# Performance work log

Hardware: AMD Instinct MI355X
Metric: run time of the kernel (lower is better)

The kernel has to match this reference:

```python
import jax, jax.numpy as jnp
import numpy as np

H = 8          # n_channels
NEIGHBORS = 5


def setup_inputs() -> dict:
    key = jax.random.key(0)
    k1, k2 = jax.random.split(key)
    B, N, C = 8, 1024, 256
    x = jax.random.normal(k1, (B, N, C), dtype=jnp.float32)
    # torch Linear weight: [out_features, in_features] = [2*H*C, C]
    W_qk = jax.random.normal(k2, (2 * H * C, C), dtype=jnp.float32) * (C ** -0.5)
    return {"x": x, "W_qk": W_qk}


def _forward(x, W_qk):
    B, N, C = x.shape
    scale = C ** -0.5
    qk = (x @ W_qk.T).reshape(B, N, 2, H, C).transpose(2, 0, 3, 1, 4)
    q, k = qk[0], qk[1]                              # [B,H,N,C]
    attn = jax.nn.softmax(jnp.einsum('bhnc,bhmc->bhnm', q, k) * scale, axis=-1)

    # clip(): top-k on detached channel-summed attention
    sum_edge = jnp.sum(jax.lax.stop_gradient(attn), axis=1)   # [B,N,N]
    _, index = jax.lax.top_k(sum_edge, NEIGHBORS)             # [B,N,NEIGHBORS]
    # Faithful to source: every mask row gets 1 at the union of ALL rows'
    # top-k indices (inner loop iterates over all rows of `inds`), plus eye(N).
    flat_idx = index.reshape(B, N * NEIGHBORS)                # [B, N*nb]
    col_mask = jnp.zeros((B, N), dtype=attn.dtype).at[
        jnp.arange(B)[:, None], flat_idx].set(1.0)            # [B,N]
    mask = jnp.maximum(jnp.eye(N, dtype=attn.dtype)[None], col_mask[:, None, :])  # [B,N,N]

    new_edge = mask[:, None] * attn                           # [B,H,N,N]

    # norm_edge(): row norm, then col norm, then row @ col^T
    norm_row = new_edge / (jnp.sum(new_edge, axis=-1, keepdims=True) + 1e-16)
    norm_col = norm_row / (jnp.sum(norm_row, axis=-2, keepdims=True) + 1e-16)
    return jnp.einsum('bhnm,bhkm->bhnk', norm_row, norm_col)  # [B,H,N,N]


def reference(x, W_qk):
    return _forward(x, W_qk)
```

## Files before the change

kernel.cpp:

```cpp
#include <hip/hip_runtime.h>
#include <hip/hip_bf16.h>
#include <cstdint>
#include <cstddef>

#define BB 8
#define HH 8
#define NN 1024
#define CC 256
#define OUTCH 4096

typedef __attribute__((ext_vector_type(8))) __bf16 bf16x8;
typedef __attribute__((ext_vector_type(4))) __bf16 bf16x4;
typedef __attribute__((ext_vector_type(4))) float f32x4;

__device__ inline void async16(const void* g, void* l)
{
  __builtin_amdgcn_global_load_lds(
      reinterpret_cast<const __attribute__((address_space(1))) unsigned int*>(
          reinterpret_cast<uintptr_t>(g)),
      reinterpret_cast<__attribute__((address_space(3))) unsigned int*>(
          reinterpret_cast<uintptr_t>(l)),
      16, 0, 0);
}

__device__ inline float waveMax(float v) {
#pragma unroll
  for (int o = 32; o > 0; o >>= 1) v = fmaxf(v, __shfl_xor(v, o, 64));
  return v;
}
__device__ inline float waveSum(float v) {
#pragma unroll
  for (int o = 32; o > 0; o >>= 1) v += __shfl_xor(v, o, 64);
  return v;
}

__global__ __launch_bounds__(256) void split_kernel(const float* __restrict__ in,
                                                    __bf16* __restrict__ hi,
                                                    __bf16* __restrict__ lo, int n4)
{
  const int i = blockIdx.x * 256 + threadIdx.x;
  if (i >= n4) return;
  const float4 v = ((const float4*)in)[i];
  bf16x4 h, l;
  h.x = (__bf16)v.x; l.x = (__bf16)(v.x - (float)h.x);
  h.y = (__bf16)v.y; l.y = (__bf16)(v.y - (float)h.y);
  h.z = (__bf16)v.z; l.z = (__bf16)(v.z - (float)h.z);
  h.w = (__bf16)v.w; l.w = (__bf16)(v.w - (float)h.w);
  ((bf16x4*)hi)[i] = h;
  ((bf16x4*)lo)[i] = l;
}

__global__ __launch_bounds__(256) void xw_mfma_kernel(
    const __bf16* __restrict__ Ah, const __bf16* __restrict__ Al,
    const __bf16* __restrict__ Bh, const __bf16* __restrict__ Bl,
    __bf16* __restrict__ Chi, __bf16* __restrict__ Clo)
{
  __shared__ __bf16 AsH[128 * 32], AsL[128 * 32], BsH[128 * 32], BsL[128 * 32];

  const int tid = threadIdx.x, lane = tid & 63, wid = tid >> 6;
  const int wr = wid >> 1, wc = wid & 1;
  const int bM = blockIdx.y * 128, bN = blockIdx.x * 128;

  const int srow = wid * 16 + (lane >> 2);
  const int scol = (lane & 3) * 8;
  const __bf16* gAh = Ah + (size_t)(bM + srow) * CC + scol;
  const __bf16* gAl = Al + (size_t)(bM + srow) * CC + scol;
  const __bf16* gBh = Bh + (size_t)(bN + srow) * CC + scol;
  const __bf16* gBl = Bl + (size_t)(bN + srow) * CC + scol;
  char* lAh = (char*)AsH + wid * 16 * 64;
  char* lAl = (char*)AsL + wid * 16 * 64;
  char* lBh = (char*)BsH + wid * 16 * 64;
  char* lBl = (char*)BsL + wid * 16 * 64;

  f32x4 acc[4][4];
  const f32x4 z = {0.f, 0.f, 0.f, 0.f};
#pragma unroll
  for (int m = 0; m < 4; ++m)
#pragma unroll
    for (int n = 0; n < 4; ++n) acc[m][n] = z;

  for (int k0 = 0; k0 < CC; k0 += 32) {
    async16(gAh + k0, lAh); async16(gAh + k0 + 64 * CC, lAh + 64 * 64);
    async16(gAl + k0, lAl); async16(gAl + k0 + 64 * CC, lAl + 64 * 64);
    async16(gBh + k0, lBh); async16(gBh + k0 + 64 * CC, lBh + 64 * 64);
    async16(gBl + k0, lBl); async16(gBl + k0 + 64 * CC, lBl + 64 * 64);
    __syncthreads();

    bf16x8 ah[4], al[4], bh_[4], bl_[4];
    const int fb = (lane & 15) * 64 + (lane >> 4) * 16;
#pragma unroll
    for (int m = 0; m < 4; ++m) {
      ah[m] = *(const bf16x8*)((const char*)AsH + (wr * 64 + m * 16) * 64 + fb);
      al[m] = *(const bf16x8*)((const char*)AsL + (wr * 64 + m * 16) * 64 + fb);
    }
#pragma unroll
    for (int n = 0; n < 4; ++n) {
      bh_[n] = *(const bf16x8*)((const char*)BsH + (wc * 64 + n * 16) * 64 + fb);
      bl_[n] = *(const bf16x8*)((const char*)BsL + (wc * 64 + n * 16) * 64 + fb);
    }
#pragma unroll
    for (int m = 0; m < 4; ++m)
#pragma unroll
      for (int n = 0; n < 4; ++n) {
        acc[m][n] = __builtin_amdgcn_mfma_f32_16x16x32_bf16(al[m], bh_[n], acc[m][n], 0, 0, 0);
        acc[m][n] = __builtin_amdgcn_mfma_f32_16x16x32_bf16(ah[m], bl_[n], acc[m][n], 0, 0, 0);
        acc[m][n] = __builtin_amdgcn_mfma_f32_16x16x32_bf16(ah[m], bh_[n], acc[m][n], 0, 0, 0);
      }
    __syncthreads();
  }

  const int fr = lane & 15;
  const int fq = lane >> 4;
#pragma unroll
  for (int m = 0; m < 4; ++m) {
    const int row0 = bM + wr * 64 + m * 16 + fq * 4;
#pragma unroll
    for (int n = 0; n < 4; ++n) {
      const int col = bN + wc * 64 + n * 16 + fr;
#pragma unroll
      for (int r = 0; r < 4; ++r) {
        const float v = acc[m][n][r];
        const __bf16 h = (__bf16)v;
        const __bf16 l = (__bf16)(v - (float)h);
        Chi[(size_t)(row0 + r) * OUTCH + col] = h;
        Clo[(size_t)(row0 + r) * OUTCH + col] = l;
      }
    }
  }
}

__global__ __launch_bounds__(256) void qkt_mfma_kernel(
    const __bf16* __restrict__ Qh, const __bf16* __restrict__ Ql,
    float* __restrict__ outall)
{
  const int f = blockIdx.x;
  const int xcd = f & 7;
  const int g = f >> 3;
  const int bh = xcd + 8 * (g >> 6);
  const int tile = g & 63;
  const int b = bh >> 3, h = bh & 7;
  const size_t qoff = (size_t)b * NN * OUTCH + (size_t)h * CC;
  const size_t koff = qoff + 2048;
  float* C = outall + ((size_t)bh << 20);

  __shared__ __bf16 AsH[128 * 32], AsL[128 * 32], BsH[128 * 32], BsL[128 * 32];

  const int tid = threadIdx.x, lane = tid & 63, wid = tid >> 6;
  const int wr = wid >> 1, wc = wid & 1;
  const int bM = (tile >> 3) * 128, bN = (tile & 7) * 128;

  const int srow = wid * 16 + (lane >> 2);
  const int scol = (lane & 3) * 8;
  const __bf16* gAh = Qh + qoff + (size_t)(bM + srow) * OUTCH + scol;
  const __bf16* gAl = Ql + qoff + (size_t)(bM + srow) * OUTCH + scol;
  const __bf16* gBh = Qh + koff + (size_t)(bN + srow) * OUTCH + scol;
  const __bf16* gBl = Ql + koff + (size_t)(bN + srow) * OUTCH + scol;
  char* lAh = (char*)AsH + wid * 16 * 64;
  char* lAl = (char*)AsL + wid * 16 * 64;
  char* lBh = (char*)BsH + wid * 16 * 64;
  char* lBl = (char*)BsL + wid * 16 * 64;

  f32x4 acc[4][4];
  const f32x4 z = {0.f, 0.f, 0.f, 0.f};
#pragma unroll
  for (int m = 0; m < 4; ++m)
#pragma unroll
    for (int n = 0; n < 4; ++n) acc[m][n] = z;

  for (int k0 = 0; k0 < CC; k0 += 32) {
    async16(gAh + k0, lAh); async16(gAh + k0 + (size_t)64 * OUTCH, lAh + 64 * 64);
    async16(gAl + k0, lAl); async16(gAl + k0 + (size_t)64 * OUTCH, lAl + 64 * 64);
    async16(gBh + k0, lBh); async16(gBh + k0 + (size_t)64 * OUTCH, lBh + 64 * 64);
    async16(gBl + k0, lBl); async16(gBl + k0 + (size_t)64 * OUTCH, lBl + 64 * 64);
    __syncthreads();

    bf16x8 ah[4], al[4], bh_[4], bl_[4];
    const int fb = (lane & 15) * 64 + (lane >> 4) * 16;
#pragma unroll
    for (int m = 0; m < 4; ++m) {
      ah[m] = *(const bf16x8*)((const char*)AsH + (wr * 64 + m * 16) * 64 + fb);
      al[m] = *(const bf16x8*)((const char*)AsL + (wr * 64 + m * 16) * 64 + fb);
    }
#pragma unroll
    for (int n = 0; n < 4; ++n) {
      bh_[n] = *(const bf16x8*)((const char*)BsH + (wc * 64 + n * 16) * 64 + fb);
      bl_[n] = *(const bf16x8*)((const char*)BsL + (wc * 64 + n * 16) * 64 + fb);
    }
#pragma unroll
    for (int m = 0; m < 4; ++m)
#pragma unroll
      for (int n = 0; n < 4; ++n) {
        acc[m][n] = __builtin_amdgcn_mfma_f32_16x16x32_bf16(al[m], bh_[n], acc[m][n], 0, 0, 0);
        acc[m][n] = __builtin_amdgcn_mfma_f32_16x16x32_bf16(ah[m], bl_[n], acc[m][n], 0, 0, 0);
        acc[m][n] = __builtin_amdgcn_mfma_f32_16x16x32_bf16(ah[m], bh_[n], acc[m][n], 0, 0, 0);
      }
    __syncthreads();
  }

  const int fr = lane & 15;
  const int fq = lane >> 4;
#pragma unroll
  for (int m = 0; m < 4; ++m) {
    const int row0 = bM + wr * 64 + m * 16 + fq * 4;
#pragma unroll
    for (int n = 0; n < 4; ++n) {
      const int col = bN + wc * 64 + n * 16 + fr;
#pragma unroll
      for (int r = 0; r < 4; ++r)
        C[(size_t)(row0 + r) * NN + col] = acc[m][n][r] * 0.0625f;
    }
  }
}

__global__ __launch_bounds__(256) void softmax_se_kernel(const float* __restrict__ logits,
                                                         __bf16* __restrict__ attnb,
                                                         float* __restrict__ se)
{
  const int bn = blockIdx.x;
  const int b = bn >> 10;
  const int n = bn & 1023;
  const int t = threadIdx.x;
  const int lane = t & 63, wv = t >> 6;
  __shared__ float wred[4];
  float4 acc = make_float4(0.f, 0.f, 0.f, 0.f);

#pragma unroll 1
  for (int h = 0; h < HH; ++h) {
    const size_t rowbase = (((size_t)(b * HH + h) << 10) + n) << 10;
    const float* ar = logits + rowbase;
    __bf16* arb = attnb + rowbase;
    float4 x = *(const float4*)(ar + (t << 2));
    float mx = waveMax(fmaxf(fmaxf(x.x, x.y), fmaxf(x.z, x.w)));
    if (lane == 0) wred[wv] = mx;
    __syncthreads();
    const float M = fmaxf(fmaxf(wred[0], wred[1]), fmaxf(wred[2], wred[3]));
    __syncthreads();

    float e0 = expf(x.x - M), e1 = expf(x.y - M), e2 = expf(x.z - M), e3 = expf(x.w - M);
    float s = waveSum(e0 + e1 + e2 + e3);
    if (lane == 0) wred[wv] = s;
    __syncthreads();
    const float inv = 1.0f / (wred[0] + wred[1] + wred[2] + wred[3]);

    const float o0 = e0 * inv, o1 = e1 * inv, o2 = e2 * inv, o3 = e3 * inv;
    bf16x4 ob; ob.x = (__bf16)o0; ob.y = (__bf16)o1; ob.z = (__bf16)o2; ob.w = (__bf16)o3;
    *(bf16x4*)(arb + (t << 2)) = ob;
    acc.x += o0; acc.y += o1; acc.z += o2; acc.w += o3;
    __syncthreads();
  }
  *(float4*)(se + (size_t)bn * NN + (t << 2)) = acc;
}

__global__ __launch_bounds__(256) void topk_kernel(const float* __restrict__ se,
                                                   float* __restrict__ colmask)
{
  const int bn = blockIdx.x;
  const int b = bn >> 10;
  const int t = threadIdx.x;
  __shared__ float vals[NN];
  __shared__ unsigned long long red[256];
  const float* rowp = se + (size_t)bn * NN;
  for (int i = t; i < NN; i += 256) vals[i] = rowp[i];
  __syncthreads();

  for (int it = 0; it < 5; ++it) {
    unsigned long long best = 0ull;
    for (int i = t; i < NN; i += 256) {
      const float v = vals[i];
      if (v >= 0.f) {
        unsigned long long key =
            ((unsigned long long)__float_as_uint(v) << 32) | (unsigned)(NN - 1 - i);
        if (key > best) best = key;
      }
    }
    red[t] = best; __syncthreads();
    for (int s = 128; s > 0; s >>= 1) {
      if (t < s) red[t] = red[t] > red[t+s] ? red[t] : red[t+s];
      __syncthreads();
    }
    if (t == 0) {
      const int idx = NN - 1 - (int)(red[0] & 0xFFFFFFFFull);
      colmask[b * NN + idx] = 1.0f;
      vals[idx] = -1.0f;
    }
    __syncthreads();
  }
}

__global__ __launch_bounds__(256) void cs_rs_kernel(const __bf16* __restrict__ attnb,
                                                    const float* __restrict__ colmask,
                                                    float* __restrict__ inv_rs,
                                                    float* __restrict__ part)
{
  const int bh = blockIdx.y;
  const int b = bh >> 3;
  const int chunk = blockIdx.x;
  const int t = threadIdx.x, lane = t & 63, wv = t >> 6;
  const __bf16* ab = attnb + ((size_t)bh << 20);
  const float* cm = colmask + b * NN;
  const int c0 = lane * 16;

  float cmv[16];
#pragma unroll
  for (int q = 0; q < 4; ++q) {
    const float4 c4 = *(const float4*)(cm + c0 + q * 4);
    cmv[q*4+0] = c4.x; cmv[q*4+1] = c4.y; cmv[q*4+2] = c4.z; cmv[q*4+3] = c4.w;
  }

  float a[16];
#pragma unroll
  for (int j = 0; j < 16; ++j) a[j] = 0.f;

  const int nbase = chunk * 64 + wv * 16;
#pragma unroll 1
  for (int r = 0; r < 16; ++r) {
    const int n = nbase + r;
    const __bf16* rowp = ab + ((size_t)n << 10) + c0;
    const bf16x8 v0 = *(const bf16x8*)(rowp);
    const bf16x8 v1 = *(const bf16x8*)(rowp + 8);
    float e[16];
    float rsum = 0.f;
#pragma unroll
    for (int j = 0; j < 8; ++j) {
      const float val = ((cmv[j] != 0.f) || (c0 + j == n)) ? (float)v0[j] : 0.f;
      e[j] = val; rsum += val;
    }
#pragma unroll
    for (int j = 0; j < 8; ++j) {
      const float val = ((cmv[8+j] != 0.f) || (c0 + 8 + j == n)) ? (float)v1[j] : 0.f;
      e[8+j] = val; rsum += val;
    }
    rsum = waveSum(rsum);
    const float ir = 1.0f / (rsum + 1e-16f);
    if (lane == 0) inv_rs[bh * NN + n] = ir;
#pragma unroll
    for (int j = 0; j < 16; ++j) a[j] += e[j] * ir;
  }

  __shared__ float l[4][NN];
#pragma unroll
  for (int j = 0; j < 16; ++j) l[wv][c0 + j] = a[j];
  __syncthreads();
  const int m0 = t << 2;
  float4 o;
  o.x = l[0][m0+0] + l[1][m0+0] + l[2][m0+0] + l[3][m0+0];
  o.y = l[0][m0+1] + l[1][m0+1] + l[2][m0+1] + l[3][m0+1];
  o.z = l[0][m0+2] + l[1][m0+2] + l[2][m0+2] + l[3][m0+2];
  o.w = l[0][m0+3] + l[1][m0+3] + l[2][m0+3] + l[3][m0+3];
  *(float4*)(part + (((size_t)chunk * (BB*HH) + bh) << 10) + m0) = o;
}

__global__ __launch_bounds__(256) void cs_fin_kernel(const float* __restrict__ part,
                                                     const float* __restrict__ colmask,
                                                     float* __restrict__ isc,
                                                     float* __restrict__ sel0)
{
  const int bh = blockIdx.x;
  const int b = bh >> 3;
  const int m0 = threadIdx.x << 2;
  float a0 = 0.f, a1 = 0.f, a2 = 0.f, a3 = 0.f;
#pragma unroll
  for (int c = 0; c < 16; ++c) {
    const float4 p = *(const float4*)(part + (((size_t)c * (BB*HH) + bh) << 10) + m0);
    a0 += p.x; a1 += p.y; a2 += p.z; a3 += p.w;
  }
  float4 o;
  o.x = 1.0f / sqrtf(a0 + 1e-16f);
  o.y = 1.0f / sqrtf(a1 + 1e-16f);
  o.z = 1.0f / sqrtf(a2 + 1e-16f);
  o.w = 1.0f / sqrtf(a3 + 1e-16f);
  *(float4*)(isc + ((size_t)bh << 10) + m0) = o;
  const float4 cm = *(const float4*)(colmask + b * NN + m0);
  float4 s;
  s.x = (cm.x != 0.f) ? o.x : 0.f;
  s.y = (cm.y != 0.f) ? o.y : 0.f;
  s.z = (cm.z != 0.f) ? o.z : 0.f;
  s.w = (cm.w != 0.f) ? o.w : 0.f;
  *(float4*)(sel0 + ((size_t)bh << 10) + m0) = s;
}

__global__ __launch_bounds__(256) void ggt_mfma_kernel(const __bf16* __restrict__ attnb,
                                                       const float* __restrict__ irs,
                                                       const float* __restrict__ iscb,
                                                       const float* __restrict__ sel0b,
                                                       float* __restrict__ outall)
{
  const int f = blockIdx.x;
  const int xcd = f & 7;
  const int g = f >> 3;
  const int bh = xcd + 8 * (g / 36);
  int tt = g % 36;

  const __bf16* A = attnb + ((size_t)bh << 20);
  const float* ir = irs + bh * NN;
  const float* isc = iscb + ((size_t)bh << 10);
  const float* sel0 = sel0b + ((size_t)bh << 10);
  float* C = outall + ((size_t)bh << 20);

  int ti = 0;
#pragma unroll
  for (int r = 0; r < 8; ++r) {
    const int len = 8 - r;
    if (tt < len) { ti = r; break; }
    tt -= len;
  }
  const int tj = ti + tt;

  __shared__ __bf16 As[128 * 32];
  __shared__ __bf16 Bs[128 * 32];

  const int tid  = threadIdx.x;
  const int lane = tid & 63;
  const int wid  = tid >> 6;
  const int wr   = wid >> 1;
  const int wc   = wid & 1;
  const int bM   = ti * 128;
  const int bN   = tj * 128;

  const int srow = wid * 16 + (lane >> 2);
  const int scol = (lane & 3) * 8;

  const int rA0 = bM + srow, rA1 = bM + 64 + srow;
  const int rB0 = bN + srow, rB1 = bN + 64 + srow;
  const float irA0 = ir[rA0], irA1 = ir[rA1], irB0 = ir[rB0], irB1 = ir[rB1];

  f32x4 acc[4][4];
  const f32x4 z = {0.f, 0.f, 0.f, 0.f};
#pragma unroll
  for (int m = 0; m < 4; ++m)
#pragma unroll
    for (int n = 0; n < 4; ++n) acc[m][n] = z;

  for (int k0 = 0; k0 < NN; k0 += 32) {
    const int kc = k0 + scol;
    const float4 i0 = *(const float4*)(isc + kc);
    const float4 i1 = *(const float4*)(isc + kc + 4);
    const float4 s0 = *(const float4*)(sel0 + kc);
    const float4 s1 = *(const float4*)(sel0 + kc + 4);
    const float iv[8] = {i0.x, i0.y, i0.z, i0.w, i1.x, i1.y, i1.z, i1.w};
    const float sv[8] = {s0.x, s0.y, s0.z, s0.w, s1.x, s1.y, s1.z, s1.w};

    const bf16x8 vA0 = *(const bf16x8*)(A + ((size_t)rA0 << 10) + kc);
    const bf16x8 vA1 = *(const bf16x8*)(A + ((size_t)rA1 << 10) + kc);
    const bf16x8 vB0 = *(const bf16x8*)(A + ((size_t)rB0 << 10) + kc);
    const bf16x8 vB1 = *(const bf16x8*)(A + ((size_t)rB1 << 10) + kc);

    bf16x8 gA0, gA1, gB0, gB1;
#pragma unroll
    for (int j = 0; j < 8; ++j) {
      const int k = kc + j;
      gA0[j] = (__bf16)((float)vA0[j] * irA0 * ((k == rA0) ? iv[j] : sv[j]));
      gA1[j] = (__bf16)((float)vA1[j] * irA1 * ((k == rA1) ? iv[j] : sv[j]));
      gB0[j] = (__bf16)((float)vB0[j] * irB0 * ((k == rB0) ? iv[j] : sv[j]));
      gB1[j] = (__bf16)((float)vB1[j] * irB1 * ((k == rB1) ? iv[j] : sv[j]));
    }
    *(bf16x8*)(&As[srow * 32 + scol])        = gA0;
    *(bf16x8*)(&As[(64 + srow) * 32 + scol]) = gA1;
    *(bf16x8*)(&Bs[srow * 32 + scol])        = gB0;
    *(bf16x8*)(&Bs[(64 + srow) * 32 + scol]) = gB1;
    __syncthreads();

    bf16x8 a[4], b[4];
    const int fb = (lane & 15) * 64 + (lane >> 4) * 16;
#pragma unroll
    for (int m = 0; m < 4; ++m)
      a[m] = *(const bf16x8*)((const char*)As + (wr * 64 + m * 16) * 64 + fb);
#pragma unroll
    for (int n = 0; n < 4; ++n)
      b[n] = *(const bf16x8*)((const char*)Bs + (wc * 64 + n * 16) * 64 + fb);
#pragma unroll
    for (int m = 0; m < 4; ++m)
#pragma unroll
      for (int n = 0; n < 4; ++n)
        acc[m][n] = __builtin_amdgcn_mfma_f32_16x16x32_bf16(a[m], b[n], acc[m][n], 0, 0, 0);
    __syncthreads();
  }

  const int fr = lane & 15;
  const int fq = lane >> 4;
#pragma unroll
  for (int m = 0; m < 4; ++m) {
    const int row0 = bM + wr * 64 + m * 16 + fq * 4;
#pragma unroll
    for (int n = 0; n < 4; ++n) {
      const int col = bN + wc * 64 + n * 16 + fr;
#pragma unroll
      for (int r = 0; r < 4; ++r)
        C[(size_t)(row0 + r) * NN + col] = acc[m][n][r];
    }
  }
  if (ti != tj) {
#pragma unroll
    for (int m = 0; m < 4; ++m) {
      const int colT = bM + wr * 64 + m * 16 + fq * 4;
#pragma unroll
      for (int n = 0; n < 4; ++n) {
        const int rowT = bN + wc * 64 + n * 16 + fr;
        *(f32x4*)(C + (size_t)rowT * NN + colT) = acc[m][n];
      }
    }
  }
}

extern "C" void kernel_launch(void* const* d_in, const int* in_sizes, int n_in,
                              void* d_out, int out_size, void* d_ws, size_t ws_size,
                              hipStream_t stream)
{
  const float* x = (const float*)d_in[0];
  const float* W = (const float*)d_in[1];
  float* logits = (float*)d_out;
  char* ws = (char*)d_ws;

  __bf16* qk_hi = (__bf16*)(ws + ((size_t)0   << 20));
  __bf16* qk_lo = (__bf16*)(ws + ((size_t)64  << 20));
  __bf16* attnb = (__bf16*)(ws + ((size_t)0   << 20));
  __bf16* x_hi  = (__bf16*)(ws + ((size_t)128 << 20));
  __bf16* x_lo  = (__bf16*)(ws + ((size_t)132 << 20));
  __bf16* W_hi  = (__bf16*)(ws + ((size_t)136 << 20));
  __bf16* W_lo  = (__bf16*)(ws + ((size_t)138 << 20));
  float*  se    = (float*)(ws + ((size_t)144 << 20));
  float*  cmask = (float*)(ws + ((size_t)176 << 20));
  float*  irs   = (float*)(ws + ((size_t)177 << 20));
  float*  isc   = (float*)(ws + ((size_t)178 << 20));
  float*  sel0  = (float*)(ws + ((size_t)179 << 20));
  float*  csp   = (float*)(ws + ((size_t)180 << 20));

  hipLaunchKernelGGL(split_kernel, dim3((BB*NN*CC/4 + 255)/256), dim3(256), 0, stream,
                     x, x_hi, x_lo, BB*NN*CC/4);
  hipLaunchKernelGGL(split_kernel, dim3((OUTCH*CC/4 + 255)/256), dim3(256), 0, stream,
                     W, W_hi, W_lo, OUTCH*CC/4);

  hipLaunchKernelGGL(xw_mfma_kernel, dim3(OUTCH/128, (BB*NN)/128, 1), dim3(256), 0, stream,
                     x_hi, x_lo, W_hi, W_lo, qk_hi, qk_lo);

  hipLaunchKernelGGL(qkt_mfma_kernel, dim3(64 * 64), dim3(256), 0, stream,
                     qk_hi, qk_lo, logits);

  hipLaunchKernelGGL(softmax_se_kernel, dim3(BB*NN), dim3(256), 0, stream,
                     logits, attnb, se);

  hipMemsetAsync(cmask, 0, (size_t)BB * NN * 4, stream);
  hipLaunchKernelGGL(topk_kernel, dim3(BB*NN), dim3(256), 0, stream, se, cmask);

  hipLaunchKernelGGL(cs_rs_kernel, dim3(16, BB*HH), dim3(256), 0, stream,
                     attnb, cmask, irs, csp);
  hipLaunchKernelGGL(cs_fin_kernel, dim3(BB*HH), dim3(256), 0, stream,
                     csp, cmask, isc, sel0);

  hipLaunchKernelGGL(ggt_mfma_kernel, dim3(36 * 64), dim3(256), 0, stream,
                     attnb, irs, isc, sel0, logits);

  (void)in_sizes; (void)n_in; (void)out_size; (void)ws_size;
}
```

Measured before the change: 577.4 us.

## Materialize normalized G matrix in separate kernel and stream it into GEMM via async LDS loads

Moves the mask, row-norm and column-scale math out of the G·Gᵀ GEMM inner loop into a standalone elementwise kernel that writes a bf16 G matrix to workspace. The GEMM then loads G tiles directly into LDS with global_load_lds instead of doing register loads, float conversions and scaling per tile. This removes repeated per-tile VALU work and register pressure from the MFMA loop. The cost is an extra full pass over the 64×1024×1024 bf16 tensor: one read and one write, roughly 256 MB of memory traffic.

```diff
diff --git a/kernel.cpp b/kernel.cpp
--- a/kernel.cpp
+++ b/kernel.cpp
@@ -351,12 +351,9 @@
 }
 
 __global__ __launch_bounds__(256) void cs_fin_kernel(const float* __restrict__ part,
-                                                     const float* __restrict__ colmask,
-                                                     float* __restrict__ isc,
-                                                     float* __restrict__ sel0)
+                                                     float* __restrict__ isc)
 {
   const int bh = blockIdx.x;
-  const int b = bh >> 3;
   const int m0 = threadIdx.x << 2;
   float a0 = 0.f, a1 = 0.f, a2 = 0.f, a3 = 0.f;
 #pragma unroll
@@ -370,19 +367,33 @@
   o.z = 1.0f / sqrtf(a2 + 1e-16f);
   o.w = 1.0f / sqrtf(a3 + 1e-16f);
   *(float4*)(isc + ((size_t)bh << 10) + m0) = o;
-  const float4 cm = *(const float4*)(colmask + b * NN + m0);
-  float4 s;
-  s.x = (cm.x != 0.f) ? o.x : 0.f;
-  s.y = (cm.y != 0.f) ? o.y : 0.f;
-  s.z = (cm.z != 0.f) ? o.z : 0.f;
-  s.w = (cm.w != 0.f) ? o.w : 0.f;
-  *(float4*)(sel0 + ((size_t)bh << 10) + m0) = s;
-}
-
-__global__ __launch_bounds__(256) void ggt_mfma_kernel(const __bf16* __restrict__ attnb,
-                                                       const float* __restrict__ irs,
-                                                       const float* __restrict__ iscb,
-                                                       const float* __restrict__ sel0b,
+}
+
+__global__ __launch_bounds__(256) void g_kernel(const __bf16* __restrict__ attnb,
+                                                const float* __restrict__ colmask,
+                                                const float* __restrict__ inv_rs,
+                                                const float* __restrict__ isc,
+                                                __bf16* __restrict__ Gb)
+{
+  const size_t idx = ((size_t)blockIdx.x * 256 + threadIdx.x) << 2;
+  const size_t row = idx >> 10;
+  const int m = (int)(idx & 1023);
+  const int n = (int)(row & 1023);
+  const int bh = (int)(row >> 10);
+  const int b = bh >> 3;
+  const bf16x4 vb = *(const bf16x4*)(attnb + idx);
+  const float4 c = *(const float4*)(colmask + b * NN + m);
+  const float4 s = *(const float4*)(isc + ((size_t)bh << 10) + m);
+  const float ir = inv_rs[row];
+  bf16x4 o;
+  o.x = (__bf16)((((c.x != 0.f) || (m + 0 == n)) ? (float)vb.x : 0.f) * ir * s.x);
+  o.y = (__bf16)((((c.y != 0.f) || (m + 1 == n)) ? (float)vb.y : 0.f) * ir * s.y);
+  o.z = (__bf16)((((c.z != 0.f) || (m + 2 == n)) ? (float)vb.z : 0.f) * ir * s.z);
+  o.w = (__bf16)((((c.w != 0.f) || (m + 3 == n)) ? (float)vb.w : 0.f) * ir * s.w);
+  *(bf16x4*)(Gb + idx) = o;
+}
+
+__global__ __launch_bounds__(256) void ggt_mfma_kernel(const __bf16* __restrict__ Gball,
                                                        float* __restrict__ outall)
 {
   const int f = blockIdx.x;
@@ -391,10 +402,7 @@
   const int bh = xcd + 8 * (g / 36);
   int tt = g % 36;
 
-  const __bf16* A = attnb + ((size_t)bh << 20);
-  const float* ir = irs + bh * NN;
-  const float* isc = iscb + ((size_t)bh << 10);
-  const float* sel0 = sel0b + ((size_t)bh << 10);
+  const __bf16* A = Gball + ((size_t)bh << 20);
   float* C = outall + ((size_t)bh << 20);
 
   int ti = 0;
@@ -419,10 +427,10 @@
 
   const int srow = wid * 16 + (lane >> 2);
   const int scol = (lane & 3) * 8;
-
-  const int rA0 = bM + srow, rA1 = bM + 64 + srow;
-  const int rB0 = bN + srow, rB1 = bN + 64 + srow;
-  const float irA0 = ir[rA0], irA1 = ir[rA1], irB0 = ir[rB0], irB1 = ir[rB1];
+  const __bf16* gA = A + (size_t)(bM + srow) * NN + scol;
+  const __bf16* gB = A + (size_t)(bN + srow) * NN + scol;
+  char* lA = (char*)As + wid * 16 * 64;
+  char* lB = (char*)Bs + wid * 16 * 64;
 
   f32x4 acc[4][4];
   const f32x4 z = {0.f, 0.f, 0.f, 0.f};
@@ -432,32 +440,10 @@
     for (int n = 0; n < 4; ++n) acc[m][n] = z;
 
   for (int k0 = 0; k0 < NN; k0 += 32) {
-    const int kc = k0 + scol;
-    const float4 i0 = *(const float4*)(isc + kc);
-    const float4 i1 = *(const float4*)(isc + kc + 4);
-    const float4 s0 = *(const float4*)(sel0 + kc);
-    const float4 s1 = *(const float4*)(sel0 + kc + 4);
-    const float iv[8] = {i0.x, i0.y, i0.z, i0.w, i1.x, i1.y, i1.z, i1.w};
-    const float sv[8] = {s0.x, s0.y, s0.z, s0.w, s1.x, s1.y, s1.z, s1.w};
-
-    const bf16x8 vA0 = *(const bf16x8*)(A + ((size_t)rA0 << 10) + kc);
-    const bf16x8 vA1 = *(const bf16x8*)(A + ((size_t)rA1 << 10) + kc);
-    const bf16x8 vB0 = *(const bf16x8*)(A + ((size_t)rB0 << 10) + kc);
-    const bf16x8 vB1 = *(const bf16x8*)(A + ((size_t)rB1 << 10) + kc);
-
-    bf16x8 gA0, gA1, gB0, gB1;
-#pragma unroll
-    for (int j = 0; j < 8; ++j) {
-      const int k = kc + j;
-      gA0[j] = (__bf16)((float)vA0[j] * irA0 * ((k == rA0) ? iv[j] : sv[j]));
-      gA1[j] = (__bf16)((float)vA1[j] * irA1 * ((k == rA1) ? iv[j] : sv[j]));
-      gB0[j] = (__bf16)((float)vB0[j] * irB0 * ((k == rB0) ? iv[j] : sv[j]));
-      gB1[j] = (__bf16)((float)vB1[j] * irB1 * ((k == rB1) ? iv[j] : sv[j]));
-    }
-    *(bf16x8*)(&As[srow * 32 + scol])        = gA0;
-    *(bf16x8*)(&As[(64 + srow) * 32 + scol]) = gA1;
-    *(bf16x8*)(&Bs[srow * 32 + scol])        = gB0;
-    *(bf16x8*)(&Bs[(64 + srow) * 32 + scol]) = gB1;
+    async16(gA + k0,           lA);
+    async16(gA + k0 + 64 * NN, lA + 64 * 64);
+    async16(gB + k0,           lB);
+    async16(gB + k0 + 64 * NN, lB + 64 * 64);
     __syncthreads();
 
     bf16x8 a[4], b[4];
@@ -522,8 +508,8 @@
   float*  cmask = (float*)(ws + ((size_t)176 << 20));
   float*  irs   = (float*)(ws + ((size_t)177 << 20));
   float*  isc   = (float*)(ws + ((size_t)178 << 20));
-  float*  sel0  = (float*)(ws + ((size_t)179 << 20));
   float*  csp   = (float*)(ws + ((size_t)180 << 20));
+  __bf16* Gb    = (__bf16*)(ws + ((size_t)192 << 20));
 
   hipLaunchKernelGGL(split_kernel, dim3((BB*NN*CC/4 + 255)/256), dim3(256), 0, stream,
                      x, x_hi, x_lo, BB*NN*CC/4);
@@ -544,11 +530,13 @@
 
   hipLaunchKernelGGL(cs_rs_kernel, dim3(16, BB*HH), dim3(256), 0, stream,
                      attnb, cmask, irs, csp);
-  hipLaunchKernelGGL(cs_fin_kernel, dim3(BB*HH), dim3(256), 0, stream,
-                     csp, cmask, isc, sel0);
+  hipLaunchKernelGGL(cs_fin_kernel, dim3(BB*HH), dim3(256), 0, stream, csp, isc);
+
+  hipLaunchKernelGGL(g_kernel, dim3((BB*HH*NN*(long long)NN) / 4 / 256), dim3(256), 0, stream,
+                     attnb, cmask, irs, isc, Gb);
 
   hipLaunchKernelGGL(ggt_mfma_kernel, dim3(36 * 64), dim3(256), 0, stream,
-                     attnb, irs, isc, sel0, logits);
+                     Gb, logits);
 
   (void)in_sizes; (void)n_in; (void)out_size; (void)ws_size;
 }
```

After: 561.3 us. 1.03x faster.
